# Kernel tuning notes

Measured on AMD Instinct MI355X. Metric: run time of the kernel, lower is better.

## Reference

```python
import jax, jax.numpy as jnp
import numpy as np

B, T, C, H = 8, 1024, 1024, 16
NEG = -1000000000.0
EPS = 1e-12


def setup_inputs() -> dict:
    key = jax.random.key(0)
    ks = jax.random.split(key, 12)
    s = 0.02  # keep pre-softmax logits in a sane range
    return {
        "x": jax.random.normal(ks[0], (B, T, C), jnp.float32),
        "mask": jax.random.randint(ks[1], (B, T), 0, 2, jnp.int32),
        "Wq": jax.random.normal(ks[2], (C, C), jnp.float32) * s,
        "bq": jax.random.normal(ks[3], (C,), jnp.float32) * s,
        "Wk": jax.random.normal(ks[4], (C, C), jnp.float32) * s,
        "bk": jax.random.normal(ks[5], (C,), jnp.float32) * s,
        "Wv": jax.random.normal(ks[6], (C, C), jnp.float32) * s,
        "bv": jax.random.normal(ks[7], (C,), jnp.float32) * s,
        "Wp": jax.random.normal(ks[8], (C, C), jnp.float32) * s,
        "bp": jax.random.normal(ks[9], (C,), jnp.float32) * s,
        "ln_w": jnp.ones((C,), jnp.float32),
        "ln_b": jnp.zeros((C,), jnp.float32),
    }


def reference(x, mask, Wq, bq, Wk, bk, Wv, bv, Wp, bp, ln_w, ln_b):
    Bx, Tx, Cx = x.shape
    hd = Cx // H
    # torch nn.Linear: y = x @ W.T + b
    def lin(inp, W, b):
        return inp @ W.T + b

    def split_heads(t):  # [B,T,C] -> [B,H,T,hd]
        return t.reshape(Bx, Tx, H, hd).transpose(0, 2, 1, 3)

    q = split_heads(lin(x, Wq, bq))
    k = split_heads(lin(x, Wk, bk))
    v = split_heads(lin(x, Wv, bv))

    att = jnp.einsum("bhqd,bhkd->bhqk", q, k) * (1.0 / jnp.sqrt(jnp.float32(hd)))
    # mask [B,T] masks key positions; broadcast to [B,1,1,T]
    att = jnp.where(mask[:, None, None, :] == 0, NEG, att)
    # stable softmax (manual max-subtract, matching original)
    att = jax.nn.softmax(att, axis=-1)
    # dropout prob 0.0 -> identity (eval-mode faithful)
    y = jnp.einsum("bhqk,bhkd->bhqd", att, v)
    y = y.transpose(0, 2, 1, 3).reshape(Bx, Tx, Cx)
    y = lin(y, Wp, bp)
    # residual + LayerNorm(eps=1e-12)
    z = y + x
    mu = jnp.mean(z, axis=-1, keepdims=True)
    var = jnp.mean(jnp.square(z - mu), axis=-1, keepdims=True)
    out = (z - mu) * jax.lax.rsqrt(var + EPS) * ln_w + ln_b
    return out
```

## Files before the change

kernel.cpp:

```cpp
#include <hip/hip_runtime.h>
#include <stdint.h>

#define B_ 8
#define T_ 1024
#define C_ 1024
#define H_ 16
#define HD 64
#define M_TOT (B_ * T_)

using f32x4 = __attribute__((ext_vector_type(4))) float;
using s16x8 = __attribute__((ext_vector_type(8))) short;
using i32x4 = __attribute__((ext_vector_type(4))) int;

__device__ __forceinline__ unsigned short f2bf(float f) {
  unsigned int u = __builtin_bit_cast(unsigned int, f);
  unsigned int r = (u + 0x7fffu + ((u >> 16) & 1u)) >> 16;
  return (unsigned short)r;
}

__device__ __forceinline__ void gload_lds16(const void* g, void* l) {
  __builtin_amdgcn_global_load_lds(
      (const __attribute__((address_space(1))) unsigned int*)g,
      (__attribute__((address_space(3))) unsigned int*)l, 16, 0, 0);
}

__global__ __launch_bounds__(256) void k_convert(
    const float* __restrict__ x, const float* __restrict__ wq,
    const float* __restrict__ wk, const float* __restrict__ wv,
    const float* __restrict__ wp, const float* __restrict__ bq,
    const float* __restrict__ bk, const float* __restrict__ bv,
    const int* __restrict__ maskp, unsigned short* __restrict__ xb,
    unsigned short* __restrict__ wqkv, unsigned short* __restrict__ wpb,
    float* __restrict__ bias_cat, unsigned int* __restrict__ mpair) {
  const long n_x = (long)M_TOT * C_;
  const long W_ELT = (long)C_ * C_;
  const long total4 = (n_x + 4 * W_ELT) >> 2;
  for (long i4 = (long)blockIdx.x * blockDim.x + threadIdx.x; i4 < total4;
       i4 += (long)gridDim.x * blockDim.x) {
    long i = i4 << 2;
    const float* src;
    unsigned short* dst;
    if (i < n_x) {
      src = x + i;
      dst = xb + i;
    } else {
      long off = i - n_x;
      int which = (int)(off >> 20);
      long wo = off & (W_ELT - 1);
      if (which < 3) {
        src = (which == 0 ? wq : which == 1 ? wk : wv) + wo;
        dst = wqkv + which * W_ELT + wo;
      } else {
        src = wp + wo;
        dst = wpb + wo;
      }
    }
    float4 v = *(const float4*)src;
    ushort4 u;
    u.x = f2bf(v.x); u.y = f2bf(v.y); u.z = f2bf(v.z); u.w = f2bf(v.w);
    *(ushort4*)dst = u;
  }
  int t = blockIdx.x * blockDim.x + threadIdx.x;
  if (t < 3 * C_) {
    float v = t < C_ ? bq[t] : (t < 2 * C_ ? bk[t - C_] : bv[t - 2 * C_]);
    bias_cat[t] = v;
  }
  if (t < B_ * T_ / 2) {
    const int* mr = maskp + t * 2;
    mpair[t] = (mr[0] ? 0xFFFFu : 0u) | (mr[1] ? 0xFFFF0000u : 0u);
  }
}

template <int EPI>
__global__ __launch_bounds__(512, 2) void k_gemm(
    const unsigned short* __restrict__ A, const unsigned short* __restrict__ Bm,
    const float* __restrict__ bias, unsigned short* __restrict__ q_ws,
    unsigned short* __restrict__ k_ws, unsigned short* __restrict__ vt_ws,
    const float* __restrict__ xres, float* __restrict__ zout) {
  __shared__ unsigned short Al[2][256 * 64];
  __shared__ unsigned short Bl[2][128 * 64];
  const int tid = threadIdx.x, lane = tid & 63, w = tid >> 6;
  const int lc = lane & 15, lr = lane >> 4;
  const int wm = w >> 1, wn = w & 1;
  const int GX = (EPI == 0) ? 24 : 8;
  const int NWG = GX * 32;
  int flat = blockIdx.y * GX + blockIdx.x;
  int swz = (flat & 7) * (NWG / 8) + (flat >> 3);
  const int m0 = (swz / GX) * 256, n0 = (swz % GX) * 128;
  const char* Ab = (const char*)A;
  const char* Bb = (const char*)Bm;

  f32x4 acc[4][4] = {};

  auto stage = [&](int buf, int kt) {
#pragma unroll
    for (int i = 0; i < 4; ++i) {
      int g = i * 512 + tid;
      int row = g >> 3, gr = g & 7;
      gload_lds16(Ab + (long)(m0 + row) * 2048 + kt * 128 + ((gr ^ (row & 7)) << 4),
                  (char*)Al[buf] + (i * 512 + w * 64) * 16);
    }
#pragma unroll
    for (int i = 0; i < 2; ++i) {
      int g = i * 512 + tid;
      int row = g >> 3, gr = g & 7;
      gload_lds16(Bb + (long)(n0 + row) * 2048 + kt * 128 + ((gr ^ (row & 7)) << 4),
                  (char*)Bl[buf] + (i * 512 + w * 64) * 16);
    }
  };

  stage(0, 0);
  asm volatile("s_waitcnt vmcnt(0)" ::: "memory");
  __builtin_amdgcn_s_barrier();
  __builtin_amdgcn_sched_barrier(0);

  int cur = 0;
  for (int kt = 0; kt < C_ / 64; ++kt) {
    if (kt + 1 < C_ / 64) stage(cur ^ 1, kt + 1);
    const char* Ac = (const char*)Al[cur];
    const char* Bc = (const char*)Bl[cur];
#pragma unroll
    for (int ks = 0; ks < 2; ++ks) {
      s16x8 af[4], bfv[4];
#pragma unroll
      for (int mf = 0; mf < 4; ++mf) {
        int ar = wm * 64 + mf * 16 + lc;
        af[mf] = *(const s16x8*)(Ac + ar * 128 + (((ks * 4 + lr) ^ (ar & 7)) << 4));
      }
#pragma unroll
      for (int nf = 0; nf < 4; ++nf) {
        int br = wn * 64 + nf * 16 + lc;
        bfv[nf] = *(const s16x8*)(Bc + br * 128 + (((ks * 4 + lr) ^ (br & 7)) << 4));
      }
#pragma unroll
      for (int mf = 0; mf < 4; ++mf)
#pragma unroll
        for (int nf = 0; nf < 4; ++nf)
          acc[mf][nf] = __builtin_amdgcn_mfma_f32_16x16x32_bf16(af[mf], bfv[nf],
                                                                acc[mf][nf], 0, 0, 0);
    }
    asm volatile("s_waitcnt vmcnt(0)" ::: "memory");
    __builtin_amdgcn_s_barrier();
    __builtin_amdgcn_sched_barrier(0);
    cur ^= 1;
  }

  if (EPI == 0) {
#pragma unroll
    for (int mf = 0; mf < 4; ++mf)
#pragma unroll
      for (int nf = 0; nf < 4; ++nf) {
        int gn = n0 + wn * 64 + nf * 16 + lc;
        int which = gn >> 10, nn = gn & 1023;
        int hh = nn >> 6, dd = nn & 63;
        float bia = bias[gn];
        if (which == 2) {
          int gm = m0 + wm * 64 + mf * 16 + lr * 4;
          int bb = gm >> 10, tt = gm & 1023;
          ushort4 pk;
          pk.x = f2bf(acc[mf][nf][0] + bia);
          pk.y = f2bf(acc[mf][nf][1] + bia);
          pk.z = f2bf(acc[mf][nf][2] + bia);
          pk.w = f2bf(acc[mf][nf][3] + bia);
          *(ushort4*)&vt_ws[((long)(bb * H_ + hh) * HD + dd) * T_ + tt] = pk;
        } else {
          unsigned short* dst = (which == 0) ? q_ws : k_ws;
          float scl = (which == 0) ? 0.18033688011112042f : 1.0f;
#pragma unroll
          for (int i = 0; i < 4; ++i) {
            int gm = m0 + wm * 64 + mf * 16 + lr * 4 + i;
            int bb = gm >> 10, tt = gm & 1023;
            dst[((long)(bb * H_ + hh) * T_ + tt) * HD + dd] =
                f2bf((acc[mf][nf][i] + bia) * scl);
          }
        }
      }
  } else {
#pragma unroll
    for (int mf = 0; mf < 4; ++mf)
#pragma unroll
      for (int nf = 0; nf < 4; ++nf) {
        int gn = n0 + wn * 64 + nf * 16 + lc;
        float bia = bias[gn];
#pragma unroll
        for (int i = 0; i < 4; ++i) {
          int gm = m0 + wm * 64 + mf * 16 + lr * 4 + i;
          long idx = (long)gm * C_ + gn;
          zout[idx] = acc[mf][nf][i] + bia + xres[idx];
        }
      }
  }
}

__global__ __launch_bounds__(512, 4) void k_attn(
    const unsigned short* __restrict__ Qp, const unsigned short* __restrict__ Kp,
    const unsigned short* __restrict__ Vtp, const unsigned int* __restrict__ mpairp,
    unsigned short* __restrict__ Yp) {
  __shared__ unsigned short Kl[2][64 * 64];
  __shared__ unsigned short Vl[2][64 * 64];
  const int tid = threadIdx.x, lane = tid & 63, w = tid >> 6;
  const int bid = blockIdx.x;
  const int xcd = bid & 7, slot = bid >> 3;
  const int bh = xcd * 16 + (slot >> 3);
  const int qt = slot & 7;
  const int b = bh >> 4, h = bh & 15;
  const int lc = lane & 15, lr = lane >> 4;
  const int q0 = qt * 128 + w * 16;

  const unsigned short* qbase = Qp + ((long)bh * T_ + q0) * HD;
  s16x8 aq0 = *(const s16x8*)(qbase + lc * HD + lr * 8);
  s16x8 aq1 = *(const s16x8*)(qbase + lc * HD + 32 + lr * 8);

  s16x8 ones;
#pragma unroll
  for (int j = 0; j < 8; ++j) ones[j] = (short)0x3F80;

  f32x4 o[4] = {};
  f32x4 o_l = {};

  const char* kb_g = (const char*)(Kp + (long)bh * T_ * HD);
  const char* vb_g = (const char*)(Vtp + (long)bh * HD * T_);
  const unsigned int* mrow2 = mpairp + b * (T_ / 2);

  auto stage = [&](int buf, int kt) {
    int f = tid * 16;
    int row = f >> 7;
    int swz = (f & 127) ^ ((row & 7) << 4);
    gload_lds16(kb_g + (long)kt * 8192 + (f & ~127) + swz,
                (char*)Kl[buf] + w * 1024);
    gload_lds16(vb_g + (long)row * (T_ * 2) + kt * 128 + swz,
                (char*)Vl[buf] + w * 1024);
  };

  stage(0, 0);
  __syncthreads();

  const int s01 = lc + ((lane & 16) << 1);
  const int s23 = s01 + 16;
  const bool hi = (lane >= 32);

  int cur = 0;
  for (int kt = 0; kt < T_ / 64; ++kt) {
    if (kt + 1 < T_ / 64) stage(cur ^ 1, kt + 1);

    f32x4 s[4];
    const char* kl = (const char*)Kl[cur];
#pragma unroll
    for (int kf = 0; kf < 4; ++kf) {
      int key = kf * 16 + lc;
      s16x8 kb0 = *(const s16x8*)(kl + ((key * 128 + lr * 16) ^ ((key & 7) << 4)));
      s16x8 kb1 = *(const s16x8*)(kl + ((key * 128 + 64 + lr * 16) ^ ((key & 7) << 4)));
      f32x4 z = {};
      z = __builtin_amdgcn_mfma_f32_16x16x32_bf16(kb0, aq0, z, 0, 0, 0);
      z = __builtin_amdgcn_mfma_f32_16x16x32_bf16(kb1, aq1, z, 0, 0, 0);
      s[kf] = z;
    }

    unsigned int mw[4][2];
#pragma unroll
    for (int kf = 0; kf < 4; ++kf) {
      mw[kf][0] = mrow2[kt * 32 + kf * 8 + lr * 2];
      mw[kf][1] = mrow2[kt * 32 + kf * 8 + lr * 2 + 1];
    }

    unsigned int pk[4][2];
#pragma unroll
    for (int kf = 0; kf < 4; ++kf) {
      float p0 = __builtin_amdgcn_exp2f(s[kf][0]);
      float p1 = __builtin_amdgcn_exp2f(s[kf][1]);
      float p2 = __builtin_amdgcn_exp2f(s[kf][2]);
      float p3 = __builtin_amdgcn_exp2f(s[kf][3]);
      unsigned int u0 = __builtin_bit_cast(unsigned int, p0);
      unsigned int u1 = __builtin_bit_cast(unsigned int, p1);
      unsigned int u2 = __builtin_bit_cast(unsigned int, p2);
      unsigned int u3 = __builtin_bit_cast(unsigned int, p3);
      pk[kf][0] = ((u1 & 0xFFFF0000u) | (u0 >> 16)) & mw[kf][0];
      pk[kf][1] = ((u3 & 0xFFFF0000u) | (u2 >> 16)) & mw[kf][1];
    }

    s16x8 ap[2];
#pragma unroll
    for (int kc = 0; kc < 2; ++kc) {
      unsigned int A0 = pk[kc * 2][0], A1 = pk[kc * 2][1];
      unsigned int B0 = pk[kc * 2 + 1][0], B1 = pk[kc * 2 + 1][1];
      unsigned int w0a = __shfl((int)A0, s01, 64), w0b = __shfl((int)B0, s01, 64);
      unsigned int w1a = __shfl((int)A1, s01, 64), w1b = __shfl((int)B1, s01, 64);
      unsigned int w2a = __shfl((int)A0, s23, 64), w2b = __shfl((int)B0, s23, 64);
      unsigned int w3a = __shfl((int)A1, s23, 64), w3b = __shfl((int)B1, s23, 64);
      i32x4 wv;
      wv[0] = (int)(hi ? w0b : w0a);
      wv[1] = (int)(hi ? w1b : w1a);
      wv[2] = (int)(hi ? w2b : w2a);
      wv[3] = (int)(hi ? w3b : w3a);
      ap[kc] = __builtin_bit_cast(s16x8, wv);
    }

#pragma unroll
    for (int kc = 0; kc < 2; ++kc) {
      int koff = kc * 64 + lr * 16;
      o_l = __builtin_amdgcn_mfma_f32_16x16x32_bf16(ones, ap[kc], o_l, 0, 0, 0);
#pragma unroll
      for (int nf = 0; nf < 4; ++nf) {
        int drow = nf * 16 + lc;
        s16x8 vb = *(const s16x8*)((const char*)Vl[cur] +
                                   ((drow * 128 + koff) ^ ((drow & 7) << 4)));
        o[nf] = __builtin_amdgcn_mfma_f32_16x16x32_bf16(vb, ap[kc], o[nf], 0, 0, 0);
      }
    }
    __syncthreads();
    cur ^= 1;
  }

  float rl = 1.0f / o_l[0];
  unsigned short* yrow = Yp + ((long)(b * T_ + q0 + lc)) * C_ + h * 64;
#pragma unroll
  for (int nf = 0; nf < 4; ++nf) {
    ushort4 pw;
    pw.x = f2bf(o[nf][0] * rl);
    pw.y = f2bf(o[nf][1] * rl);
    pw.z = f2bf(o[nf][2] * rl);
    pw.w = f2bf(o[nf][3] * rl);
    *(ushort4*)(yrow + nf * 16 + lr * 4) = pw;
  }
}

__global__ __launch_bounds__(256) void k_ln(const float* __restrict__ z,
                                            const float* __restrict__ lw,
                                            const float* __restrict__ lb,
                                            float* __restrict__ out) {
  const int row = blockIdx.x;
  float4 v = ((const float4*)(z + (long)row * C_))[threadIdx.x];
  float s = v.x + v.y + v.z + v.w;
  float s2 = v.x * v.x + v.y * v.y + v.z * v.z + v.w * v.w;
#pragma unroll
  for (int d = 1; d < 64; d <<= 1) {
    s += __shfl_xor(s, d, 64);
    s2 += __shfl_xor(s2, d, 64);
  }
  __shared__ float rs[4], rq[4];
  int wv_ = threadIdx.x >> 6;
  if ((threadIdx.x & 63) == 0) { rs[wv_] = s; rq[wv_] = s2; }
  __syncthreads();
  s = rs[0] + rs[1] + rs[2] + rs[3];
  s2 = rq[0] + rq[1] + rq[2] + rq[3];
  float mu = s * (1.0f / C_);
  float var = s2 * (1.0f / C_) - mu * mu;
  float inv = rsqrtf(var + 1e-12f);
  float4 wv4 = ((const float4*)lw)[threadIdx.x];
  float4 bv4 = ((const float4*)lb)[threadIdx.x];
  float4 ov;
  ov.x = (v.x - mu) * inv * wv4.x + bv4.x;
  ov.y = (v.y - mu) * inv * wv4.y + bv4.y;
  ov.z = (v.z - mu) * inv * wv4.z + bv4.z;
  ov.w = (v.w - mu) * inv * wv4.w + bv4.w;
  ((float4*)(out + (long)row * C_))[threadIdx.x] = ov;
}

extern "C" void kernel_launch(void* const* d_in, const int* in_sizes, int n_in,
                              void* d_out, int out_size, void* d_ws,
                              size_t ws_size, hipStream_t stream) {
  const float* x = (const float*)d_in[0];
  const int* mask = (const int*)d_in[1];
  const float* Wq = (const float*)d_in[2];
  const float* bq = (const float*)d_in[3];
  const float* Wk = (const float*)d_in[4];
  const float* bk = (const float*)d_in[5];
  const float* Wv = (const float*)d_in[6];
  const float* bv = (const float*)d_in[7];
  const float* Wp = (const float*)d_in[8];
  const float* bp = (const float*)d_in[9];
  const float* lnw = (const float*)d_in[10];
  const float* lnb = (const float*)d_in[11];
  float* out = (float*)d_out;

  char* ws = (char*)d_ws;
  const size_t MB = 1024 * 1024;
  unsigned short* xb = (unsigned short*)(ws);
  unsigned short* q_ws = (unsigned short*)(ws + 16 * MB);
  unsigned short* k_ws = (unsigned short*)(ws + 32 * MB);
  unsigned short* vt_ws = (unsigned short*)(ws + 48 * MB);
  unsigned short* y_ws = (unsigned short*)(ws + 64 * MB);
  unsigned short* wqkv = (unsigned short*)(ws + 80 * MB);
  unsigned short* wpb = (unsigned short*)(ws + 86 * MB);
  float* bias_cat = (float*)(ws + 88 * MB);
  unsigned int* mpair = (unsigned int*)(ws + 88 * MB + 16384);
  float* z = (float*)(ws);

  k_convert<<<dim3(2048), dim3(256), 0, stream>>>(x, Wq, Wk, Wv, Wp, bq, bk, bv,
                                                  mask, xb, wqkv, wpb, bias_cat,
                                                  mpair);
  k_gemm<0><<<dim3(24, 32), dim3(512), 0, stream>>>(
      xb, wqkv, bias_cat, q_ws, k_ws, vt_ws, nullptr, nullptr);
  k_attn<<<dim3(1024), dim3(512), 0, stream>>>(q_ws, k_ws, vt_ws, mpair, y_ws);
  k_gemm<1><<<dim3(8, 32), dim3(512), 0, stream>>>(
      y_ws, wpb, bp, nullptr, nullptr, nullptr, x, z);
  k_ln<<<dim3(8192), dim3(256), 0, stream>>>(z, lnw, lnb, out);
}
```

Measured before the change: 190.0 us.

## Shrink GEMM tiles to 128x128 and prefetch two K-stages ahead

The GEMM workgroup drops from 512 to 256 threads with a 128x128 output tile (previously 256x128), which doubles the grid. The main loop is rewritten to issue global-to-LDS loads two K-steps ahead, using partial vmcnt waits instead of draining everything each step. It also splits each K-step into two halves so the refill of the free buffer overlaps the second half's MFMAs, and raises wave priority around those MFMAs. The goals are more workgroups for occupancy and less load latency exposed at barriers, at the cost of less operand reuse per tile and an extra barrier per iteration.

```diff
diff --git a/kernel.cpp b/kernel.cpp
--- a/kernel.cpp
+++ b/kernel.cpp
@@ -72,21 +72,21 @@
 }
 
 template <int EPI>
-__global__ __launch_bounds__(512, 2) void k_gemm(
+__global__ __launch_bounds__(256, 2) void k_gemm(
     const unsigned short* __restrict__ A, const unsigned short* __restrict__ Bm,
     const float* __restrict__ bias, unsigned short* __restrict__ q_ws,
     unsigned short* __restrict__ k_ws, unsigned short* __restrict__ vt_ws,
     const float* __restrict__ xres, float* __restrict__ zout) {
-  __shared__ unsigned short Al[2][256 * 64];
+  __shared__ unsigned short Al[2][128 * 64];
   __shared__ unsigned short Bl[2][128 * 64];
   const int tid = threadIdx.x, lane = tid & 63, w = tid >> 6;
   const int lc = lane & 15, lr = lane >> 4;
   const int wm = w >> 1, wn = w & 1;
   const int GX = (EPI == 0) ? 24 : 8;
-  const int NWG = GX * 32;
+  const int NWG = GX * 64;
   int flat = blockIdx.y * GX + blockIdx.x;
   int swz = (flat & 7) * (NWG / 8) + (flat >> 3);
-  const int m0 = (swz / GX) * 256, n0 = (swz % GX) * 128;
+  const int m0 = (swz / GX) * 128, n0 = (swz % GX) * 128;
   const char* Ab = (const char*)A;
   const char* Bb = (const char*)Bm;
 
@@ -95,54 +95,80 @@
   auto stage = [&](int buf, int kt) {
 #pragma unroll
     for (int i = 0; i < 4; ++i) {
-      int g = i * 512 + tid;
+      int g = i * 256 + tid;
       int row = g >> 3, gr = g & 7;
       gload_lds16(Ab + (long)(m0 + row) * 2048 + kt * 128 + ((gr ^ (row & 7)) << 4),
-                  (char*)Al[buf] + (i * 512 + w * 64) * 16);
-    }
-#pragma unroll
-    for (int i = 0; i < 2; ++i) {
-      int g = i * 512 + tid;
+                  (char*)Al[buf] + (i * 256 + w * 64) * 16);
+    }
+#pragma unroll
+    for (int i = 0; i < 4; ++i) {
+      int g = i * 256 + tid;
       int row = g >> 3, gr = g & 7;
       gload_lds16(Bb + (long)(n0 + row) * 2048 + kt * 128 + ((gr ^ (row & 7)) << 4),
-                  (char*)Bl[buf] + (i * 512 + w * 64) * 16);
+                  (char*)Bl[buf] + (i * 256 + w * 64) * 16);
     }
   };
 
   stage(0, 0);
-  asm volatile("s_waitcnt vmcnt(0)" ::: "memory");
+  stage(1, 1);
+  asm volatile("s_waitcnt vmcnt(8)" ::: "memory");
+  __builtin_amdgcn_sched_barrier(0);
   __builtin_amdgcn_s_barrier();
   __builtin_amdgcn_sched_barrier(0);
 
-  int cur = 0;
-  for (int kt = 0; kt < C_ / 64; ++kt) {
-    if (kt + 1 < C_ / 64) stage(cur ^ 1, kt + 1);
+#pragma unroll
+  for (int kt = 0; kt < 16; ++kt) {
+    const int cur = kt & 1;
     const char* Ac = (const char*)Al[cur];
     const char* Bc = (const char*)Bl[cur];
-#pragma unroll
-    for (int ks = 0; ks < 2; ++ks) {
-      s16x8 af[4], bfv[4];
-#pragma unroll
-      for (int mf = 0; mf < 4; ++mf) {
-        int ar = wm * 64 + mf * 16 + lc;
-        af[mf] = *(const s16x8*)(Ac + ar * 128 + (((ks * 4 + lr) ^ (ar & 7)) << 4));
-      }
-#pragma unroll
-      for (int nf = 0; nf < 4; ++nf) {
-        int br = wn * 64 + nf * 16 + lc;
-        bfv[nf] = *(const s16x8*)(Bc + br * 128 + (((ks * 4 + lr) ^ (br & 7)) << 4));
-      }
-#pragma unroll
-      for (int mf = 0; mf < 4; ++mf)
-#pragma unroll
-        for (int nf = 0; nf < 4; ++nf)
-          acc[mf][nf] = __builtin_amdgcn_mfma_f32_16x16x32_bf16(af[mf], bfv[nf],
-                                                                acc[mf][nf], 0, 0, 0);
-    }
-    asm volatile("s_waitcnt vmcnt(0)" ::: "memory");
+    s16x8 af0[4], bf0[4];
+#pragma unroll
+    for (int mf = 0; mf < 4; ++mf) {
+      int ar = wm * 64 + mf * 16 + lc;
+      af0[mf] = *(const s16x8*)(Ac + ar * 128 + ((lr ^ (ar & 7)) << 4));
+    }
+#pragma unroll
+    for (int nf = 0; nf < 4; ++nf) {
+      int br = wn * 64 + nf * 16 + lc;
+      bf0[nf] = *(const s16x8*)(Bc + br * 128 + ((lr ^ (br & 7)) << 4));
+    }
+#pragma unroll
+    for (int mf = 0; mf < 4; ++mf)
+#pragma unroll
+      for (int nf = 0; nf < 4; ++nf)
+        acc[mf][nf] = __builtin_amdgcn_mfma_f32_16x16x32_bf16(af0[mf], bf0[nf],
+                                                              acc[mf][nf], 0, 0, 0);
+    s16x8 af1[4], bf1[4];
+#pragma unroll
+    for (int mf = 0; mf < 4; ++mf) {
+      int ar = wm * 64 + mf * 16 + lc;
+      af1[mf] = *(const s16x8*)(Ac + ar * 128 + (((4 + lr) ^ (ar & 7)) << 4));
+    }
+#pragma unroll
+    for (int nf = 0; nf < 4; ++nf) {
+      int br = wn * 64 + nf * 16 + lc;
+      bf1[nf] = *(const s16x8*)(Bc + br * 128 + (((4 + lr) ^ (br & 7)) << 4));
+    }
+    asm volatile("s_waitcnt lgkmcnt(0)" ::: "memory");
+    __builtin_amdgcn_sched_barrier(0);
     __builtin_amdgcn_s_barrier();
     __builtin_amdgcn_sched_barrier(0);
-    cur ^= 1;
+    if (kt + 2 < 16) stage(cur, kt + 2);
+    __builtin_amdgcn_s_setprio(1);
+#pragma unroll
+    for (int mf = 0; mf < 4; ++mf)
+#pragma unroll
+      for (int nf = 0; nf < 4; ++nf)
+        acc[mf][nf] = __builtin_amdgcn_mfma_f32_16x16x32_bf16(af1[mf], bf1[nf],
+                                                              acc[mf][nf], 0, 0, 0);
+    __builtin_amdgcn_s_setprio(0);
+    if (kt + 2 < 16)
+      asm volatile("s_waitcnt vmcnt(8)" ::: "memory");
+    else
+      asm volatile("s_waitcnt vmcnt(0)" ::: "memory");
+    __builtin_amdgcn_sched_barrier(0);
+    __builtin_amdgcn_s_barrier();
+    __builtin_amdgcn_sched_barrier(0);
   }
 
   if (EPI == 0) {
@@ -389,10 +415,10 @@
   k_convert<<<dim3(2048), dim3(256), 0, stream>>>(x, Wq, Wk, Wv, Wp, bq, bk, bv,
                                                   mask, xb, wqkv, wpb, bias_cat,
                                                   mpair);
-  k_gemm<0><<<dim3(24, 32), dim3(512), 0, stream>>>(
+  k_gemm<0><<<dim3(24, 64), dim3(256), 0, stream>>>(
       xb, wqkv, bias_cat, q_ws, k_ws, vt_ws, nullptr, nullptr);
   k_attn<<<dim3(1024), dim3(512), 0, stream>>>(q_ws, k_ws, vt_ws, mpair, y_ws);
-  k_gemm<1><<<dim3(8, 32), dim3(512), 0, stream>>>(
+  k_gemm<1><<<dim3(8, 64), dim3(256), 0, stream>>>(
       y_ws, wpb, bp, nullptr, nullptr, nullptr, x, z);
   k_ln<<<dim3(8192), dim3(256), 0, stream>>>(z, lnw, lnb, out);
 }
```

New measurement: 176.2 us. 1.08x faster.
